# Kernel tuning notes

Measured on AMD Instinct MI355X. Metric: run time of the kernel, lower is better.

## Reference

```python
import jax, jax.numpy as jnp
import numpy as np

B, S, H, F, E, TOPK = 2, 2048, 1024, 2048, 8, 2


def setup_inputs() -> dict:
    key = jax.random.key(0)
    k1, k2, k3, k4, k5 = jax.random.split(key, 5)
    scale_h = 1.0 / np.sqrt(H)
    scale_f = 1.0 / np.sqrt(F)
    return {
        "hidden_states": jax.random.normal(k1, (B, S, H), dtype=jnp.float32),
        "gate_w": jax.random.normal(k2, (E, H), dtype=jnp.float32) * scale_h,
        "w1": jax.random.normal(k3, (E, F, H), dtype=jnp.float32) * scale_h,
        "w2": jax.random.normal(k4, (E, H, F), dtype=jnp.float32) * scale_f,
        "w3": jax.random.normal(k5, (E, F, H), dtype=jnp.float32) * scale_h,
    }


def reference(hidden_states, gate_w, w1, w2, w3):
    b, s, h = hidden_states.shape
    x = hidden_states.reshape(-1, h)                      # [T, H]
    T = x.shape[0]
    router_logits = x @ gate_w.T                          # [T, E]
    probs = jax.nn.softmax(router_logits.astype(jnp.float32), axis=-1)
    rw, sel = jax.lax.top_k(probs, TOPK)                  # [T, k]
    rw = rw / jnp.sum(rw, axis=-1, keepdims=True)
    rw = rw.astype(x.dtype)
    # combine weights [T, E]: routing weight where selected, else 0
    combine = jnp.zeros((T, E), dtype=x.dtype).at[
        jnp.arange(T)[:, None], sel].add(rw)
    # dense dispatch: compute every expert on all tokens, mask via combine
    h1 = jnp.einsum('th,efh->etf', x, w1)                 # [E, T, F]
    h3 = jnp.einsum('th,efh->etf', x, w3)
    gated = jax.nn.silu(h1) * h3
    out_e = jnp.einsum('etf,ehf->eth', gated, w2)         # [E, T, H]
    final = jnp.einsum('eth,te->th', out_e, combine)      # [T, H]
    return final.reshape(b, s, h), router_logits
```

## Files before the change

kernel.cpp:

```cpp
#include <hip/hip_runtime.h>
#include <hip/hip_bf16.h>

#define TT 4096
#define HH 1024
#define FF 2048
#define EE 8
#define NC32 2048
#define LDSU 32768

typedef short short8_t __attribute__((ext_vector_type(8)));
typedef float f32x4 __attribute__((ext_vector_type(4)));

__device__ __forceinline__ unsigned short f2b(float f) {
  union { float f; unsigned u; } v; v.f = f;
  return (unsigned short)((v.u + 0x7fffu + ((v.u >> 16) & 1u)) >> 16);
}

__device__ __forceinline__ void gload16(const unsigned short* g, void* l) {
  __builtin_amdgcn_global_load_lds(
      (const __attribute__((address_space(1))) void*)g,
      (__attribute__((address_space(3))) void*)l, 16, 0, 0);
}

#define FENCE asm volatile("" ::: "memory")

__device__ __forceinline__ void conv_ilp(const float* __restrict__ src,
                                         unsigned short* __restrict__ dst,
                                         int c, int tid) {
  size_t base = (size_t)c * 8192 + tid * 4;
  float4 v[8];
#pragma unroll
  for (int j = 0; j < 8; ++j)
    v[j] = *reinterpret_cast<const float4*>(src + base + j * 1024);
#pragma unroll
  for (int j = 0; j < 8; ++j) {
    ushort4 b4;
    b4.x = f2b(v[j].x); b4.y = f2b(v[j].y); b4.z = f2b(v[j].z); b4.w = f2b(v[j].w);
    *reinterpret_cast<ushort4*>(dst + base + j * 1024) = b4;
  }
}

__global__ __launch_bounds__(256) void front_kernel(
    const float* __restrict__ x, const float* __restrict__ gw,
    const float* __restrict__ w1, const float* __restrict__ w3,
    const float* __restrict__ w2,
    float* __restrict__ out_logits,
    unsigned short* __restrict__ xbf,
    unsigned short* __restrict__ w1bf, unsigned short* __restrict__ w3bf,
    unsigned short* __restrict__ w2bf,
    int* __restrict__ sel01, float2* __restrict__ w01)
{
  int tid = threadIdx.x;
  int b = blockIdx.x;
  if (b >= TT) {
    int cb = b - TT;
    if (cb < NC32)          conv_ilp(w1, w1bf, cb, tid);
    else if (cb < 2 * NC32) conv_ilp(w3, w3bf, cb - NC32, tid);
    else                    conv_ilp(w2, w2bf, cb - 2 * NC32, tid);
    return;
  }
  int t = b;

  __shared__ float xs[HH];
  __shared__ float lg[EE];

  float4 v = reinterpret_cast<const float4*>(x + (size_t)t * HH)[tid];
  xs[tid * 4 + 0] = v.x; xs[tid * 4 + 1] = v.y;
  xs[tid * 4 + 2] = v.z; xs[tid * 4 + 3] = v.w;
  ushort4 b4;
  b4.x = f2b(v.x); b4.y = f2b(v.y); b4.z = f2b(v.z); b4.w = f2b(v.w);
  reinterpret_cast<ushort4*>(xbf + (size_t)t * HH)[tid] = b4;
  __syncthreads();

  int lane = tid & 63, wv = tid >> 6;
  for (int e = wv; e < EE; e += 4) {
    float s = 0.f;
    const float* g = gw + (size_t)e * HH;
#pragma unroll
    for (int j = 0; j < HH / 64; ++j) s += xs[lane + j * 64] * g[lane + j * 64];
#pragma unroll
    for (int off = 32; off > 0; off >>= 1) s += __shfl_down(s, off);
    if (lane == 0) lg[e] = s;
  }
  __syncthreads();

  if (tid < 8) out_logits[(size_t)t * EE + tid] = lg[tid];
  if (tid == 0) {
    float l[EE];
#pragma unroll
    for (int e = 0; e < EE; ++e) l[e] = lg[e];
    int e0 = 0;
#pragma unroll
    for (int e = 1; e < EE; ++e) if (l[e] > l[e0]) e0 = e;
    int e1 = -1;
#pragma unroll
    for (int e = 0; e < EE; ++e) if (e != e0 && (e1 < 0 || l[e] > l[e1])) e1 = e;
    float p1 = expf(l[e1] - l[e0]);
    float w0 = 1.f / (1.f + p1);
    float w1v = p1 * w0;
    sel01[t] = e0 | (e1 << 8);
    w01[t] = make_float2(w0, w1v);
  }
}

__global__ __launch_bounds__(256) void build_kernel(
    const int* __restrict__ sel01, const float2* __restrict__ w01,
    int* __restrict__ counts, int* __restrict__ tokidx, float* __restrict__ rww)
{
  int e = blockIdx.x;
  int tid = threadIdx.x, lane = tid & 63, wv = tid >> 6;
  __shared__ int wsum[4];
  int base = 0;
  for (int t0 = 0; t0 < TT; t0 += 256) {
    int t = t0 + tid;
    int s = sel01[t];
    int e0 = s & 255, e1 = (s >> 8) & 255;
    bool hit = (e0 == e) || (e1 == e);
    float w = 0.f;
    if (hit) { float2 ww = w01[t]; w = (e0 == e) ? ww.x : ww.y; }
    unsigned long long m = __ballot(hit);
    int wpre = __popcll(m & ((1ull << lane) - 1));
    if (lane == 63) wsum[wv] = wpre + (hit ? 1 : 0);
    __syncthreads();
    int wbase = base;
    for (int q = 0; q < wv; ++q) wbase += wsum[q];
    if (hit) {
      int pos = wbase + wpre;
      tokidx[e * TT + pos] = t;
      rww[e * TT + pos] = w;
    }
    base += wsum[0] + wsum[1] + wsum[2] + wsum[3];
    __syncthreads();
  }
  if (tid == 0) counts[e] = base;
}

__global__ __launch_bounds__(256) void conv_kernel(
    const float* __restrict__ src, unsigned short* __restrict__ dst)
{
  conv_ilp(src, dst, blockIdx.x, threadIdx.x);
}

__global__ __launch_bounds__(256) void combine_kernel(
    const float4* __restrict__ s0, const float4* __restrict__ s1,
    float4* __restrict__ out)
{
  size_t i = (size_t)blockIdx.x * 256 + threadIdx.x;
  float4 a = s0[i], b = s1[i];
  float4 r;
  r.x = a.x + b.x; r.y = a.y + b.y; r.z = a.z + b.z; r.w = a.w + b.w;
  out[i] = r;
}

__global__ __launch_bounds__(256) void up_gate_kernel(
    const unsigned short* __restrict__ xbf,
    const unsigned short* __restrict__ w1bf, const unsigned short* __restrict__ w3bf,
    const int* __restrict__ counts, const int* __restrict__ tokidx,
    unsigned short* __restrict__ gated)
{
  int e = blockIdx.z;
  int n = counts[e];
  int row0 = blockIdx.y * 128;
  if (row0 >= n) return;
  int fbase = blockIdx.x * 64;

  int pe = 0;
  for (int q = 0; q < e; ++q) pe += (counts[q] + 127) & ~127;

  __shared__ __align__(16) char lds[2 * LDSU];

  int tid = threadIdx.x;
  int lane = tid & 63, wv = tid >> 6;
  int sb = (tid & 7) ^ ((tid >> 3) & 7);

  const unsigned short* ga[4];
#pragma unroll
  for (int j = 0; j < 4; ++j) {
    int r = min(row0 + (tid >> 3) + 32 * j, n - 1);
    ga[j] = xbf + (size_t)tokidx[e * TT + r] * HH + sb * 8;
  }
  const unsigned short* gb1[2];
  const unsigned short* gb3[2];
#pragma unroll
  for (int j = 0; j < 2; ++j) {
    size_t rw_ = (size_t)e * FF + fbase + (tid >> 3) + 32 * j;
    gb1[j] = w1bf + rw_ * HH + sb * 8;
    gb3[j] = w3bf + rw_ * HH + sb * 8;
  }

  int wr = (wv >> 1) * 64, wc = (wv & 1) * 32;
  int fr = lane & 15, kq = lane >> 4, l7 = lane & 7;

  f32x4 acc1[4][2], acc3[4][2];
#pragma unroll
  for (int m = 0; m < 4; ++m)
#pragma unroll
    for (int nn = 0; nn < 2; ++nn) { acc1[m][nn] = (f32x4)0.f; acc3[m][nn] = (f32x4)0.f; }

#define UG_STAGE(T, SOFF) do {                                                     \
    _Pragma("unroll") for (int j = 0; j < 4; ++j)                                  \
      gload16(ga[j] + (T) * 64, lds + (SOFF) + j * 4096 + wv * 1024);              \
    _Pragma("unroll") for (int j = 0; j < 2; ++j) {                                \
      gload16(gb1[j] + (T) * 64, lds + (SOFF) + 16384 + j * 4096 + wv * 1024);     \
      gload16(gb3[j] + (T) * 64, lds + (SOFF) + 24576 + j * 4096 + wv * 1024);     \
    } } while (0)

#define UG_PHASE(SOFF, KS) do {                                                             \
    int bswz = (((KS) * 4 + kq) ^ l7) * 16;                                                 \
    short8_t a[4], b1f[2], b3f[2];                                                          \
    _Pragma("unroll") for (int m = 0; m < 4; ++m)                                           \
      a[m] = *(const short8_t*)(lds + (SOFF) + (wr + m * 16 + fr) * 128 + bswz);            \
    _Pragma("unroll") for (int nn = 0; nn < 2; ++nn) {                                      \
      b1f[nn] = *(const short8_t*)(lds + (SOFF) + 16384 + (wc + nn * 16 + fr) * 128 + bswz); \
      b3f[nn] = *(const short8_t*)(lds + (SOFF) + 24576 + (wc + nn * 16 + fr) * 128 + bswz); \
    }                                                                                       \
    __builtin_amdgcn_s_setprio(1);                                                          \
    _Pragma("unroll") for (int m = 0; m < 4; ++m)                                           \
      _Pragma("unroll") for (int nn = 0; nn < 2; ++nn) {                                    \
        acc1[m][nn] = __builtin_amdgcn_mfma_f32_16x16x32_bf16(a[m], b1f[nn], acc1[m][nn], 0, 0, 0); \
        acc3[m][nn] = __builtin_amdgcn_mfma_f32_16x16x32_bf16(a[m], b3f[nn], acc3[m][nn], 0, 0, 0); \
      }                                                                                     \
    __builtin_amdgcn_s_setprio(0);                                                          \
  } while (0)

#define UG_NT 16
#define UG_ITER(T, SOFF) do {                                          \
    if ((T) < UG_NT - 1) asm volatile("s_waitcnt vmcnt(8)" ::: "memory"); \
    else                 asm volatile("s_waitcnt vmcnt(0)" ::: "memory"); \
    __builtin_amdgcn_s_barrier(); FENCE;                               \
    UG_PHASE(SOFF, 0);                                                 \
    FENCE; __builtin_amdgcn_s_barrier(); FENCE;                        \
    UG_PHASE(SOFF, 1);                                                 \
    FENCE; __builtin_amdgcn_s_barrier(); FENCE;                        \
    if ((T) + 2 < UG_NT) UG_STAGE((T) + 2, SOFF);                      \
  } while (0)

  UG_STAGE(0, 0);
  UG_STAGE(1, LDSU);
  for (int t2 = 0; t2 < UG_NT; t2 += 2) { UG_ITER(t2, 0); UG_ITER(t2 + 1, LDSU); }
#undef UG_STAGE
#undef UG_PHASE
#undef UG_ITER

  size_t gbase = ((size_t)pe + row0) * FF + fbase;
#pragma unroll
  for (int m = 0; m < 4; ++m) {
#pragma unroll
    for (int nn = 0; nn < 2; ++nn) {
      f32x4 h1v = acc1[m][nn], h3v = acc3[m][nn];
#pragma unroll
      for (int j = 0; j < 4; ++j) {
        float z = h1v[j];
        float val = (z / (1.f + expf(-z))) * h3v[j];
        int r = wr + m * 16 + (lane >> 4) * 4 + j;
        int c = wc + nn * 16 + fr;
        gated[gbase + (size_t)r * FF + c] = f2b(val);
      }
    }
  }
}

__global__ __launch_bounds__(256) void down_kernel(
    const unsigned short* __restrict__ gated,
    const unsigned short* __restrict__ w2bf,
    const int* __restrict__ counts, const int* __restrict__ tokidx,
    const float* __restrict__ rww, const int* __restrict__ sel01,
    float* __restrict__ slots)
{
  int e = blockIdx.z;
  int n = counts[e];
  int row0 = blockIdx.y * 128;
  if (row0 >= n) return;
  int hbase = blockIdx.x * 128;
  int valid = min(128, n - row0);

  int pe = 0;
  for (int q = 0; q < e; ++q) pe += (counts[q] + 127) & ~127;

  __shared__ __align__(16) char lds[2 * LDSU];

  int tid = threadIdx.x;
  int lane = tid & 63, wv = tid >> 6;
  int sb = (tid & 7) ^ ((tid >> 3) & 7);

  const unsigned short* ga[4];
  const unsigned short* gb[4];
#pragma unroll
  for (int j = 0; j < 4; ++j) {
    ga[j] = gated + ((size_t)pe + row0 + (tid >> 3) + 32 * j) * FF + sb * 8;
    gb[j] = w2bf + ((size_t)e * HH + hbase + (tid >> 3) + 32 * j) * FF + sb * 8;
  }

  int wr = (wv >> 1) * 64, wc = (wv & 1) * 64;
  int fr = lane & 15, kq = lane >> 4, l7 = lane & 7;

  f32x4 acc[4][4];
#pragma unroll
  for (int m = 0; m < 4; ++m)
#pragma unroll
    for (int nn = 0; nn < 4; ++nn) acc[m][nn] = (f32x4)0.f;

#define DN_STAGE(T, SOFF) do {                                                   \
    _Pragma("unroll") for (int j = 0; j < 4; ++j) {                              \
      gload16(ga[j] + (T) * 64, lds + (SOFF) + j * 4096 + wv * 1024);            \
      gload16(gb[j] + (T) * 64, lds + (SOFF) + 16384 + j * 4096 + wv * 1024);    \
    } } while (0)

#define DN_PHASE(SOFF, KS) do {                                                            \
    int bswz = (((KS) * 4 + kq) ^ l7) * 16;                                                \
    short8_t a[4], bf[4];                                                                  \
    _Pragma("unroll") for (int m = 0; m < 4; ++m)                                          \
      a[m] = *(const short8_t*)(lds + (SOFF) + (wr + m * 16 + fr) * 128 + bswz);           \
    _Pragma("unroll") for (int nn = 0; nn < 4; ++nn)                                       \
      bf[nn] = *(const short8_t*)(lds + (SOFF) + 16384 + (wc + nn * 16 + fr) * 128 + bswz); \
    __builtin_amdgcn_s_setprio(1);                                                         \
    _Pragma("unroll") for (int m = 0; m < 4; ++m)                                          \
      _Pragma("unroll") for (int nn = 0; nn < 4; ++nn)                                     \
        acc[m][nn] = __builtin_amdgcn_mfma_f32_16x16x32_bf16(a[m], bf[nn], acc[m][nn], 0, 0, 0); \
    __builtin_amdgcn_s_setprio(0);                                                         \
  } while (0)

#define DN_NT 32
#define DN_ITER(T, SOFF) do {                                          \
    if ((T) < DN_NT - 1) asm volatile("s_waitcnt vmcnt(8)" ::: "memory"); \
    else                 asm volatile("s_waitcnt vmcnt(0)" ::: "memory"); \
    __builtin_amdgcn_s_barrier(); FENCE;                               \
    DN_PHASE(SOFF, 0);                                                 \
    FENCE; __builtin_amdgcn_s_barrier(); FENCE;                        \
    DN_PHASE(SOFF, 1);                                                 \
    FENCE; __builtin_amdgcn_s_barrier(); FENCE;                        \
    if ((T) + 2 < DN_NT) DN_STAGE((T) + 2, SOFF);                      \
  } while (0)

  DN_STAGE(0, 0);
  DN_STAGE(1, LDSU);
  for (int t2 = 0; t2 < DN_NT; t2 += 2) { DN_ITER(t2, 0); DN_ITER(t2 + 1, LDSU); }
#undef DN_STAGE
#undef DN_PHASE
#undef DN_ITER

#pragma unroll
  for (int m = 0; m < 4; ++m) {
    int rbase = wr + m * 16 + (lane >> 4) * 4;
#pragma unroll
    for (int j = 0; j < 4; ++j) {
      int r = rbase + j;
      if (r < valid) {
        int t = tokidx[e * TT + row0 + r];
        float w = rww[e * TT + row0 + r];
        int sl = ((sel01[t] & 255) == e) ? 0 : 1;
        float* dst = slots + (size_t)sl * TT * HH + (size_t)t * HH;
#pragma unroll
        for (int nn = 0; nn < 4; ++nn) {
          int c = hbase + wc + nn * 16 + fr;
          dst[c] = w * acc[m][nn][j];
        }
      }
    }
  }
}

extern "C" void kernel_launch(void* const* d_in, const int* in_sizes, int n_in,
                              void* d_out, int out_size, void* d_ws, size_t ws_size,
                              hipStream_t stream) {
  const float* x  = (const float*)d_in[0];
  const float* gw = (const float*)d_in[1];
  const float* w1 = (const float*)d_in[2];
  const float* w2 = (const float*)d_in[3];
  const float* w3 = (const float*)d_in[4];

  float* final_out  = (float*)d_out;
  float* out_logits = final_out + (size_t)TT * HH;

  char* ws = (char*)d_ws;
  int*    counts = (int*)(ws + 0);
  int*    sel01  = (int*)(ws + 1024);
  float2* w01    = (float2*)(ws + 20480);
  int*    tokidx = (int*)(ws + 53248);
  float*  rww    = (float*)(ws + 184320);
  unsigned short* xbf   = (unsigned short*)(ws + 315392);
  unsigned short* w1bf  = (unsigned short*)(ws + 8704000);
  unsigned short* w3bf  = (unsigned short*)(ws + 42258432);
  unsigned short* gated = (unsigned short*)(ws + 75812864);
  const size_t base_end = 113561600;
  bool big = ws_size >= base_end + 33554432;
  unsigned short* w2bf = big ? (unsigned short*)(ws + base_end) : w1bf;
  float* slots = (float*)w3bf;

  int nconvblk = (big ? 3 : 2) * NC32;
  front_kernel<<<TT + nconvblk, 256, 0, stream>>>(
      x, gw, w1, w3, w2, out_logits, xbf, w1bf, w3bf, w2bf, sel01, w01);
  build_kernel<<<EE, 256, 0, stream>>>(sel01, w01, counts, tokidx, rww);
  up_gate_kernel<<<dim3(FF / 64, TT / 128, EE), 256, 0, stream>>>(
      xbf, w1bf, w3bf, counts, tokidx, gated);
  if (!big) conv_kernel<<<NC32, 256, 0, stream>>>(w2, w1bf);
  down_kernel<<<dim3(HH / 128, TT / 128, EE), 256, 0, stream>>>(
      gated, w2bf, counts, tokidx, rww, sel01, slots);
  combine_kernel<<<TT * HH / 1024, 256, 0, stream>>>(
      (const float4*)slots, (const float4*)(slots + (size_t)TT * HH),
      (float4*)final_out);
}
```

Baseline: 251.9 us.

## Software-pipeline LDS fragment reads against MFMA in both expert GEMM loops

Restructures the main loops of the up/gate and down-projection kernels so LDS fragment reads for the next k-substep are issued before the MFMAs of the current one, using double-buffered register fragments. Barriers drop from three per tile to one per tile, with a full lgkmcnt/vmcnt drain before each. This aims to hide LDS latency and barrier stalls behind matrix math. The cost is higher register pressure, which may lower occupancy, and waiting on all outstanding global loads at each barrier may expose memory latency.

```diff
diff --git a/kernel.cpp b/kernel.cpp
--- a/kernel.cpp
+++ b/kernel.cpp
@@ -197,6 +197,9 @@
 #pragma unroll
     for (int nn = 0; nn < 2; ++nn) { acc1[m][nn] = (f32x4)0.f; acc3[m][nn] = (f32x4)0.f; }
 
+  short8_t a0[4], b10[2], b30[2];
+  short8_t a1[4], b11[2], b31[2];
+
 #define UG_STAGE(T, SOFF) do {                                                     \
     _Pragma("unroll") for (int j = 0; j < 4; ++j)                                  \
       gload16(ga[j] + (T) * 64, lds + (SOFF) + j * 4096 + wv * 1024);              \
@@ -205,42 +208,56 @@
       gload16(gb3[j] + (T) * 64, lds + (SOFF) + 24576 + j * 4096 + wv * 1024);     \
     } } while (0)
 
-#define UG_PHASE(SOFF, KS) do {                                                             \
+#define UG_READS(SOFF, KS, A_, B1_, B3_) do {                                               \
     int bswz = (((KS) * 4 + kq) ^ l7) * 16;                                                 \
-    short8_t a[4], b1f[2], b3f[2];                                                          \
     _Pragma("unroll") for (int m = 0; m < 4; ++m)                                           \
-      a[m] = *(const short8_t*)(lds + (SOFF) + (wr + m * 16 + fr) * 128 + bswz);            \
+      A_[m] = *(const short8_t*)(lds + (SOFF) + (wr + m * 16 + fr) * 128 + bswz);           \
     _Pragma("unroll") for (int nn = 0; nn < 2; ++nn) {                                      \
-      b1f[nn] = *(const short8_t*)(lds + (SOFF) + 16384 + (wc + nn * 16 + fr) * 128 + bswz); \
-      b3f[nn] = *(const short8_t*)(lds + (SOFF) + 24576 + (wc + nn * 16 + fr) * 128 + bswz); \
-    }                                                                                       \
+      B1_[nn] = *(const short8_t*)(lds + (SOFF) + 16384 + (wc + nn * 16 + fr) * 128 + bswz); \
+      B3_[nn] = *(const short8_t*)(lds + (SOFF) + 24576 + (wc + nn * 16 + fr) * 128 + bswz); \
+    } } while (0)
+
+#define UG_MFMA(A_, B1_, B3_) do {                                                          \
     __builtin_amdgcn_s_setprio(1);                                                          \
     _Pragma("unroll") for (int m = 0; m < 4; ++m)                                           \
       _Pragma("unroll") for (int nn = 0; nn < 2; ++nn) {                                    \
-        acc1[m][nn] = __builtin_amdgcn_mfma_f32_16x16x32_bf16(a[m], b1f[nn], acc1[m][nn], 0, 0, 0); \
-        acc3[m][nn] = __builtin_amdgcn_mfma_f32_16x16x32_bf16(a[m], b3f[nn], acc3[m][nn], 0, 0, 0); \
+        acc1[m][nn] = __builtin_amdgcn_mfma_f32_16x16x32_bf16(A_[m], B1_[nn], acc1[m][nn], 0, 0, 0); \
+        acc3[m][nn] = __builtin_amdgcn_mfma_f32_16x16x32_bf16(A_[m], B3_[nn], acc3[m][nn], 0, 0, 0); \
       }                                                                                     \
     __builtin_amdgcn_s_setprio(0);                                                          \
   } while (0)
 
+#define UG_WAITS do {                                                  \
+    asm volatile("s_waitcnt lgkmcnt(0) vmcnt(0)" ::: "memory");        \
+    __builtin_amdgcn_sched_barrier(0);                                 \
+    __builtin_amdgcn_s_barrier(); FENCE;                               \
+  } while (0)
+
 #define UG_NT 16
-#define UG_ITER(T, SOFF) do {                                          \
-    if ((T) < UG_NT - 1) asm volatile("s_waitcnt vmcnt(8)" ::: "memory"); \
-    else                 asm volatile("s_waitcnt vmcnt(0)" ::: "memory"); \
-    __builtin_amdgcn_s_barrier(); FENCE;                               \
-    UG_PHASE(SOFF, 0);                                                 \
-    FENCE; __builtin_amdgcn_s_barrier(); FENCE;                        \
-    UG_PHASE(SOFF, 1);                                                 \
-    FENCE; __builtin_amdgcn_s_barrier(); FENCE;                        \
-    if ((T) + 2 < UG_NT) UG_STAGE((T) + 2, SOFF);                      \
-  } while (0)
-
   UG_STAGE(0, 0);
   UG_STAGE(1, LDSU);
-  for (int t2 = 0; t2 < UG_NT; t2 += 2) { UG_ITER(t2, 0); UG_ITER(t2 + 1, LDSU); }
+  asm volatile("s_waitcnt vmcnt(8)" ::: "memory");
+  __builtin_amdgcn_s_barrier(); FENCE;
+  UG_READS(0, 0, a0, b10, b30);
+
+  for (int t2 = 0; t2 < UG_NT; t2 += 2) {
+    UG_READS(0, 1, a1, b11, b31);
+    UG_MFMA(a0, b10, b30);
+    UG_WAITS;
+    if (t2 + 2 < UG_NT) UG_STAGE(t2 + 2, 0);
+    UG_READS(LDSU, 0, a0, b10, b30);
+    UG_MFMA(a1, b11, b31);
+    UG_READS(LDSU, 1, a1, b11, b31);
+    UG_MFMA(a0, b10, b30);
+    UG_WAITS;
+    if (t2 + 3 < UG_NT) UG_STAGE(t2 + 3, LDSU);
+    if (t2 + 2 < UG_NT) UG_READS(0, 0, a0, b10, b30);
+    UG_MFMA(a1, b11, b31);
+  }
 #undef UG_STAGE
-#undef UG_PHASE
-#undef UG_ITER
+#undef UG_READS
+#undef UG_MFMA
+#undef UG_WAITS
 
   size_t gbase = ((size_t)pe + row0) * FF + fbase;
 #pragma unroll
@@ -300,44 +317,63 @@
 #pragma unroll
     for (int nn = 0; nn < 4; ++nn) acc[m][nn] = (f32x4)0.f;
 
+  short8_t a0[4], bf0[4];
+  short8_t a1[4], bf1[4];
+
 #define DN_STAGE(T, SOFF) do {                                                   \
     _Pragma("unroll") for (int j = 0; j < 4; ++j) {                              \
       gload16(ga[j] + (T) * 64, lds + (SOFF) + j * 4096 + wv * 1024);            \
       gload16(gb[j] + (T) * 64, lds + (SOFF) + 16384 + j * 4096 + wv * 1024);    \
     } } while (0)
 
-#define DN_PHASE(SOFF, KS) do {                                                            \
+#define DN_READS(SOFF, KS, A_, B_) do {                                                    \
     int bswz = (((KS) * 4 + kq) ^ l7) * 16;                                                \
-    short8_t a[4], bf[4];                                                                  \
     _Pragma("unroll") for (int m = 0; m < 4; ++m)                                          \
-      a[m] = *(const short8_t*)(lds + (SOFF) + (wr + m * 16 + fr) * 128 + bswz);           \
+      A_[m] = *(const short8_t*)(lds + (SOFF) + (wr + m * 16 + fr) * 128 + bswz);          \
     _Pragma("unroll") for (int nn = 0; nn < 4; ++nn)                                       \
-      bf[nn] = *(const short8_t*)(lds + (SOFF) + 16384 + (wc + nn * 16 + fr) * 128 + bswz); \
+      B_[nn] = *(const short8_t*)(lds + (SOFF) + 16384 + (wc + nn * 16 + fr) * 128 + bswz); \
+  } while (0)
+
+#define DN_MFMA(A_, B_) do {                                                               \
     __builtin_amdgcn_s_setprio(1);                                                         \
     _Pragma("unroll") for (int m = 0; m < 4; ++m)                                          \
       _Pragma("unroll") for (int nn = 0; nn < 4; ++nn)                                     \
-        acc[m][nn] = __builtin_amdgcn_mfma_f32_16x16x32_bf16(a[m], bf[nn], acc[m][nn], 0, 0, 0); \
+        acc[m][nn] = __builtin_amdgcn_mfma_f32_16x16x32_bf16(A_[m], B_[nn], acc[m][nn], 0, 0, 0); \
     __builtin_amdgcn_s_setprio(0);                                                         \
   } while (0)
 
+#define DN_WAITS do {                                                  \
+    asm volatile("s_waitcnt lgkmcnt(0) vmcnt(0)" ::: "memory");        \
+    __builtin_amdgcn_sched_barrier(0);                                 \
+    __builtin_amdgcn_s_barrier(); FENCE;                               \
+  } while (0)
+
 #define DN_NT 32
-#define DN_ITER(T, SOFF) do {                                          \
-    if ((T) < DN_NT - 1) asm volatile("s_waitcnt vmcnt(8)" ::: "memory"); \
-    else                 asm volatile("s_waitcnt vmcnt(0)" ::: "memory"); \
-    __builtin_amdgcn_s_barrier(); FENCE;                               \
-    DN_PHASE(SOFF, 0);                                                 \
-    FENCE; __builtin_amdgcn_s_barrier(); FENCE;                        \
-    DN_PHASE(SOFF, 1);                                                 \
-    FENCE; __builtin_amdgcn_s_barrier(); FENCE;                        \
-    if ((T) + 2 < DN_NT) DN_STAGE((T) + 2, SOFF);                      \
-  } while (0)
-
   DN_STAGE(0, 0);
   DN_STAGE(1, LDSU);
-  for (int t2 = 0; t2 < DN_NT; t2 += 2) { DN_ITER(t2, 0); DN_ITER(t2 + 1, LDSU); }
+  asm volatile("s_waitcnt vmcnt(8)" ::: "memory");
+  __builtin_amdgcn_s_barrier(); FENCE;
+  DN_READS(0, 0, a0, bf0);
+
+  for (int t2 = 0; t2 < DN_NT; t2 += 2) {
+    DN_READS(0, 1, a1, bf1);
+    DN_MFMA(a0, bf0);
+    DN_WAITS;
+    if (t2 + 2 < DN_NT) DN_STAGE(t2 + 2, 0);
+    DN_READS(LDSU, 0, a0, bf0);
+    DN_MFMA(a1, bf1);
+
+    DN_READS(LDSU, 1, a1, bf1);
+    DN_MFMA(a0, bf0);
+    DN_WAITS;
+    if (t2 + 3 < DN_NT) DN_STAGE(t2 + 3, LDSU);
+    if (t2 + 2 < DN_NT) DN_READS(0, 0, a0, bf0);
+    DN_MFMA(a1, bf1);
+  }
 #undef DN_STAGE
-#undef DN_PHASE
-#undef DN_ITER
+#undef DN_READS
+#undef DN_MFMA
+#undef DN_WAITS
 
 #pragma unroll
   for (int m = 0; m < 4; ++m) {
```

New measurement: 249.5 us (median of 2 runs). No clear change (-0.9%).
